# Optimization experiments

Measured on AMD Instinct MI355X. Metric: run time of the kernel, lower is better.

Reference implementation:

```python
import jax, jax.numpy as jnp
import numpy as np

B, D_IN, D_HID, D_OUT, N_EXP, K = 32768, 256, 512, 256, 16, 2


def setup_inputs() -> dict:
    key = jax.random.key(0)
    ks = jax.random.split(key, 5)
    s_in = 1.0 / np.sqrt(D_IN)
    s_hid = 1.0 / np.sqrt(D_HID)
    return {
        "x": jax.random.normal(ks[0], (B, D_IN), jnp.float32),
        "Wg": jax.random.normal(ks[1], (D_IN, N_EXP), jnp.float32) * s_in,
        "bg": jnp.zeros((N_EXP,), jnp.float32),
        "W1": jax.random.normal(ks[2], (N_EXP, D_IN, D_HID), jnp.float32) * s_in,
        "b1": jnp.zeros((N_EXP, D_HID), jnp.float32),
        "W2": jax.random.normal(ks[3], (N_EXP, D_HID, D_OUT), jnp.float32) * s_hid,
        "b2": jnp.zeros((N_EXP, D_OUT), jnp.float32),
    }


def reference(x, Wg, bg, W1, b1, W2, b2):
    # Gating: linear -> softmax -> top-k -> renormalize (inference path, no noise)
    logits = x @ Wg + bg                       # [B, E]
    probs = jax.nn.softmax(logits, axis=-1)
    top_w, top_idx = jax.lax.top_k(probs, K)   # [B, K]
    top_w = top_w / jnp.sum(top_w, axis=-1, keepdims=True)

    # Expert MLPs (evaluate all experts densely, then gather selected outputs;
    # same math as masked gather -> MLP -> weighted scatter-add)
    h = jax.nn.relu(jnp.einsum('bi,eih->beh', x, W1) + b1[None])  # [B, E, H]
    y_all = jnp.einsum('beh,eho->beo', h, W2) + b2[None]          # [B, E, O]

    y_sel = jnp.take_along_axis(y_all, top_idx[:, :, None], axis=1)  # [B, K, O]
    return jnp.sum(y_sel * top_w[:, :, None], axis=1)                # [B, O]
```

## Files before the change

kernel.cpp:

```cpp
#include <hip/hip_runtime.h>
#include <stdint.h>

#define BTOK 32768
#define DIN 256
#define DHID 512
#define DOUT 256
#define NEXP 16
#define BM 128
#define CH 64
#define NCH 8
#define SLOTS 96

typedef __attribute__((ext_vector_type(8))) short bf16x8;
typedef __attribute__((ext_vector_type(16))) float f32x16;

__device__ __forceinline__ unsigned short f2bf(float f){
  unsigned u = __builtin_bit_cast(unsigned, f);
  u = u + 0x7FFFu + ((u >> 16) & 1u);
  return (unsigned short)(u >> 16);
}
__device__ __forceinline__ float bf2f(unsigned short h){
  return __builtin_bit_cast(float, (unsigned)h << 16);
}
__device__ __forceinline__ void gload16(const void* g, void* l){
  __builtin_amdgcn_global_load_lds((const __attribute__((address_space(1))) unsigned int*)g,
                                   (__attribute__((address_space(3))) unsigned int*)l, 16, 0, 0);
}

__global__ __launch_bounds__(256) void transpose_cvt(const float* __restrict__ src,
                                                     unsigned short* __restrict__ dst,
                                                     int R, int C){
  __shared__ float t[32][33];
  int e = blockIdx.z, r0 = blockIdx.y * 32, c0 = blockIdx.x * 32;
  int lx = threadIdx.x & 31, ly = threadIdx.x >> 5;
  const float* s = src + (size_t)e * R * C;
  unsigned short* d = dst + (size_t)e * R * C;
#pragma unroll
  for (int i = 0; i < 4; i++){ int r = ly + i * 8; t[r][lx] = s[(size_t)(r0 + r) * C + c0 + lx]; }
  __syncthreads();
#pragma unroll
  for (int i = 0; i < 4; i++){ int r = ly + i * 8; d[(size_t)(c0 + r) * R + r0 + lx] = f2bf(t[lx][r]); }
}

__global__ __launch_bounds__(256) void transpose_cvt_w2(const float* __restrict__ src,
                                                        unsigned short* __restrict__ dst){
  __shared__ float t[32][33];
  int e = blockIdx.z, r0 = blockIdx.y * 32, c0 = blockIdx.x * 32;
  int lx = threadIdx.x & 31, ly = threadIdx.x >> 5;
  const float* s = src + (size_t)e * DHID * DOUT;
  unsigned short* d = dst + (size_t)e * DHID * DOUT + (r0 >> 6) * (DOUT * CH) + (r0 & 32);
#pragma unroll
  for (int i = 0; i < 4; i++){ int r = ly + i * 8; t[r][lx] = s[(size_t)(r0 + r) * DOUT + c0 + lx]; }
  __syncthreads();
#pragma unroll
  for (int i = 0; i < 4; i++){ int rr = ly + i * 8; d[(size_t)(c0 + rr) * CH + lx] = f2bf(t[lx][rr]); }
}

__global__ __launch_bounds__(256) void gating_kernel(const float* __restrict__ x,
                                                     const float* __restrict__ Wg,
                                                     const float* __restrict__ bg,
                                                     unsigned short* __restrict__ x_bf,
                                                     int* __restrict__ top_idx,
                                                     float* __restrict__ top_w,
                                                     int* __restrict__ counts){
  __shared__ float WgT[16][256];
  __shared__ int hist[16];
  int tid = threadIdx.x;
#pragma unroll
  for (int j = 0; j < 4; j++){
    float4 wv = *(const float4*)(Wg + tid * 16 + j * 4);
    WgT[j * 4 + 0][tid] = wv.x; WgT[j * 4 + 1][tid] = wv.y;
    WgT[j * 4 + 2][tid] = wv.z; WgT[j * 4 + 3][tid] = wv.w;
  }
  if (tid < 16) hist[tid] = 0;
  __syncthreads();
  int wid = tid >> 6, lane = tid & 63;

  for (int t = 0; t < 16; t++){
    int tok = blockIdx.x * 64 + wid * 16 + t;
    const float4 xv = *(const float4*)(x + (size_t)tok * DIN + lane * 4);
    ushort4 xb; xb.x = f2bf(xv.x); xb.y = f2bf(xv.y); xb.z = f2bf(xv.z); xb.w = f2bf(xv.w);
    *(ushort4*)(x_bf + (size_t)tok * DIN + lane * 4) = xb;
    float logit[16];
#pragma unroll
    for (int e = 0; e < 16; e++){
      const float4 wv = *(const float4*)(&WgT[e][lane * 4]);
      float v = xv.x * wv.x + xv.y * wv.y + xv.z * wv.z + xv.w * wv.w;
#pragma unroll
      for (int off = 32; off; off >>= 1) v += __shfl_xor(v, off, 64);
      logit[e] = v + bg[e];
    }
    if (lane == 0){
      int i1 = 0; float v1 = logit[0];
#pragma unroll
      for (int e = 1; e < 16; e++) if (logit[e] > v1){ v1 = logit[e]; i1 = e; }
      int i2 = -1; float v2 = -3.4e38f;
#pragma unroll
      for (int e = 0; e < 16; e++) if (e != i1 && logit[e] > v2){ v2 = logit[e]; i2 = e; }
      float tt = expf(v2 - v1);
      float w1 = 1.0f / (1.0f + tt);
      float w2 = tt / (1.0f + tt);
      top_idx[tok * 2] = i1; top_idx[tok * 2 + 1] = i2;
      top_w[tok * 2] = w1;  top_w[tok * 2 + 1] = w2;
      atomicAdd(&hist[i1], 1); atomicAdd(&hist[i2], 1);
    }
  }
  __syncthreads();
  if (tid < 16) atomicAdd(&counts[tid], hist[tid]);
}

__global__ void prefix_kernel(const int* __restrict__ counts, int* __restrict__ offsets,
                              int* __restrict__ cursor, int* __restrict__ bm_e,
                              int* __restrict__ bm_start, int* __restrict__ bm_end){
  int lane = threadIdx.x & 63;
  int c = (lane < 16) ? counts[lane] : 0;
  int s = c;
#pragma unroll
  for (int off = 1; off < 16; off <<= 1){ int o = __shfl_up(s, off, 64); if (lane >= off) s += o; }
  int start = s - c;
  if (lane < 16){ offsets[lane] = start; cursor[lane] = start; }
  int nb = (c + BM - 1) >> 7;
  int nb_partner = __shfl(nb, lane ^ 8, 64);
  if (lane < 8){
    int filled = nb + nb_partner;
    if (filled > SLOTS) filled = SLOTS;
    for (int i = filled; i < SLOTS; i++) bm_e[lane * SLOTS + i] = -1;
  }
  if (lane < 16){
    int sbase = (lane < 8) ? 0 : nb_partner;
    int xcd = lane & 7;
    for (int b = 0; b < nb; b++){
      int idx = xcd * SLOTS + sbase + b;
      if (sbase + b < SLOTS){
        bm_e[idx] = lane; bm_start[idx] = start + b * BM; bm_end[idx] = start + c;
      }
    }
  }
}

__global__ __launch_bounds__(256) void scatter_kernel(const int* __restrict__ top_idx,
                                                      const float* __restrict__ top_w,
                                                      int* __restrict__ cursor,
                                                      int* __restrict__ pair_tok,
                                                      float* __restrict__ pair_w){
  __shared__ int hist[16], base[16], rank[16];
  int tid = threadIdx.x;
  if (tid < 16){ hist[tid] = 0; rank[tid] = 0; }
  __syncthreads();
  int t = blockIdx.x * 256 + tid;
  int e0 = top_idx[t * 2], e1 = top_idx[t * 2 + 1];
  float w0 = top_w[t * 2], w1 = top_w[t * 2 + 1];
  atomicAdd(&hist[e0], 1); atomicAdd(&hist[e1], 1);
  __syncthreads();
  if (tid < 16) base[tid] = atomicAdd(&cursor[tid], hist[tid]);
  __syncthreads();
  int r0 = atomicAdd(&rank[e0], 1);
  int p0 = base[e0] + r0;
  pair_tok[p0] = t; pair_w[p0] = w0;
  int r1 = atomicAdd(&rank[e1], 1);
  int p1 = base[e1] + r1;
  pair_tok[p1] = t | (1 << 16); pair_w[p1] = w1;
}

__global__ __launch_bounds__(512, 1) void moe_gemm_kernel(
    const unsigned short* __restrict__ x_bf,
    const unsigned short* __restrict__ W1t,
    const unsigned short* __restrict__ W2c,
    const float* __restrict__ b1,
    const float* __restrict__ b2,
    const int* __restrict__ pair_tok, const float* __restrict__ pair_w,
    const int* __restrict__ bm_e, const int* __restrict__ bm_start,
    const int* __restrict__ bm_end,
    unsigned short* __restrict__ ypair){
  int xcd = blockIdx.x & 7, slot = blockIdx.x >> 3;
  int bmi = xcd * SLOTS + slot;
  int e = bm_e[bmi];
  if (e < 0) return;
  int rs = bm_start[bmi], re = bm_end[bmi];

  __shared__ unsigned short w1s[2][CH * 256];
  __shared__ unsigned short w2s[2][256 * CH];
  __shared__ unsigned short hs[BM * CH];

  int tid = threadIdx.x, wid = tid >> 6, lane = tid & 63;
  int l31 = lane & 31, l5 = lane >> 5;
  int mg = wid >> 1, hg = wid & 1;
  char* hsb = (char*)hs;
  const char* gW1 = (const char*)(W1t + (size_t)e * DHID * DIN);
  const char* gW2 = (const char*)(W2c + (size_t)e * DOUT * DHID);

  int o1, o2;
  { int r = tid >> 5; o1 = r * 512 + (((tid & 31) ^ (r & 15)) * 16); }
  { int p = tid >> 4; int q = (tid & 15) ^ (p & 15);
    o2 = (p * 2 + (q >> 3)) * 128 + (q & 7) * 16; }

#define STAGE(c, sl) {                                                    \
    const char* s1 = gW1 + (size_t)(c) * 32768;                           \
    const char* s2 = gW2 + (size_t)(c) * 32768;                           \
    char* d1 = (char*)w1s[sl]; char* d2 = (char*)w2s[sl];                 \
    _Pragma("unroll")                                                     \
    for (int k = 0; k < 4; k++){                                          \
      gload16(s1 + o1 + k * 8192, d1 + tid * 16 + k * 8192);              \
      gload16(s2 + o2 + k * 8192, d2 + tid * 16 + k * 8192);              \
    } }

  bf16x8 xr[16];
  {
    int g0 = rs + mg * 32 + l31;
    int gc = g0 < re ? g0 : (re - 1);
    int tok = pair_tok[gc] & 0xFFFF;
    const unsigned short* xrow = x_bf + (size_t)tok * DIN + l5 * 8;
#pragma unroll
    for (int ks = 0; ks < 16; ks++) xr[ks] = *(const bf16x8*)(xrow + ks * 16);
  }

  const f32x16 fzero = {0.f,0.f,0.f,0.f,0.f,0.f,0.f,0.f,0.f,0.f,0.f,0.f,0.f,0.f,0.f,0.f};
  f32x16 acc[4];
  acc[0] = fzero; acc[1] = fzero; acc[2] = fzero; acc[3] = fzero;

  STAGE(0, 0);
  asm volatile("s_waitcnt vmcnt(0)" ::: "memory");
  __builtin_amdgcn_sched_barrier(0);
  __builtin_amdgcn_s_barrier();
  __builtin_amdgcn_sched_barrier(0);

  int hid = hg * 32 + l31;
  int swzA = (hid & 15) << 4;

  for (int c = 0; c < NCH; c++){
    int sl = c & 1;
    if (c + 1 < NCH) STAGE(c + 1, sl ^ 1);

    float b1v = b1[e * DHID + c * CH + hid];

    {
      const char* w1b = (const char*)w1s[sl];
      f32x16 h0 = fzero, h1 = fzero;
#pragma unroll
      for (int ks = 0; ks < 16; ks += 2){
        bf16x8 bA = *(const bf16x8*)(w1b + hid * 512 + ((ks * 32 + l5 * 16) ^ swzA));
        bf16x8 bB = *(const bf16x8*)(w1b + hid * 512 + (((ks + 1) * 32 + l5 * 16) ^ swzA));
        h0 = __builtin_amdgcn_mfma_f32_32x32x16_bf16(xr[ks], bA, h0, 0, 0, 0);
        h1 = __builtin_amdgcn_mfma_f32_32x32x16_bf16(xr[ks + 1], bB, h1, 0, 0, 0);
      }
      f32x16 hsum = h0 + h1;
      int h2 = hg * 64 + l31 * 2;
#pragma unroll
      for (int r = 0; r < 16; r++){
        int tk = mg * 32 + (r & 3) + ((r >> 2) << 3) + (l5 << 2);
        float v = fmaxf(hsum[r] + b1v, 0.f);
        int adr = (tk >> 1) * 256 + ((((tk & 1) << 7) + h2) ^ (((tk >> 1) & 15) << 4));
        *(unsigned short*)(hsb + adr) = f2bf(v);
      }
    }
    asm volatile("s_waitcnt lgkmcnt(0)" ::: "memory");
    __builtin_amdgcn_sched_barrier(0);
    __builtin_amdgcn_s_barrier();
    __builtin_amdgcn_sched_barrier(0);

    {
      const char* w2b = (const char*)w2s[sl];
      int tk = mg * 32 + l31;
      int hswz = ((tk >> 1) & 15) << 4;
      int hbase = (tk >> 1) * 256;
      int hhi = (tk & 1) << 7;
#pragma unroll
      for (int ks = 0; ks < 4; ks++){
        bf16x8 ha = *(const bf16x8*)(hsb + hbase + ((hhi + ks * 32 + l5 * 16) ^ hswz));
#pragma unroll
        for (int ot = 0; ot < 4; ot++){
          int n = hg * 128 + ot * 32 + l31;
          int adr = (n >> 1) * 256 + ((((n & 1) << 7) + ks * 32 + l5 * 16) ^ (((n >> 1) & 15) << 4));
          bf16x8 bb = *(const bf16x8*)(w2b + adr);
          acc[ot] = __builtin_amdgcn_mfma_f32_32x32x16_bf16(ha, bb, acc[ot], 0, 0, 0);
        }
      }
    }
    if (c + 1 < NCH){
      asm volatile("s_waitcnt vmcnt(0) lgkmcnt(0)" ::: "memory");
      __builtin_amdgcn_sched_barrier(0);
      __builtin_amdgcn_s_barrier();
      __builtin_amdgcn_sched_barrier(0);
    }
  }

  {
    float b2v[4];
#pragma unroll
    for (int ot = 0; ot < 4; ot++) b2v[ot] = b2[e * DOUT + hg * 128 + ot * 32 + l31];
#pragma unroll
    for (int r = 0; r < 16; r++){
      int tl = mg * 32 + (r & 3) + ((r >> 2) << 3) + (l5 << 2);
      int gg = rs + tl;
      if (gg < re){
        int pt = pair_tok[gg];
        int yrow = (pt & 0xFFFF) * 2 + (pt >> 16);
        float w = pair_w[gg];
        unsigned short* yp = ypair + (size_t)yrow * DOUT + hg * 128 + l31;
#pragma unroll
        for (int ot = 0; ot < 4; ot++)
          yp[ot * 32] = f2bf(w * (acc[ot][r] + b2v[ot]));
      }
    }
  }
#undef STAGE
}

__global__ __launch_bounds__(256) void combine_kernel(const unsigned short* __restrict__ yp,
                                                      float* __restrict__ out){
  int idx = blockIdx.x * 256 + threadIdx.x;
  int t = idx >> 6;
  int c4 = (idx & 63) << 2;
  ushort4 a = *(const ushort4*)(yp + (size_t)(t * 2) * DOUT + c4);
  ushort4 b = *(const ushort4*)(yp + (size_t)(t * 2 + 1) * DOUT + c4);
  float4 o;
  o.x = bf2f(a.x) + bf2f(b.x);
  o.y = bf2f(a.y) + bf2f(b.y);
  o.z = bf2f(a.z) + bf2f(b.z);
  o.w = bf2f(a.w) + bf2f(b.w);
  *(float4*)(out + (size_t)t * DOUT + c4) = o;
}

extern "C" void kernel_launch(void* const* d_in, const int* in_sizes, int n_in,
                              void* d_out, int out_size, void* d_ws, size_t ws_size,
                              hipStream_t stream){
  (void)in_sizes; (void)n_in; (void)out_size; (void)ws_size;
  const float* x  = (const float*)d_in[0];
  const float* Wg = (const float*)d_in[1];
  const float* bg = (const float*)d_in[2];
  const float* W1 = (const float*)d_in[3];
  const float* b1 = (const float*)d_in[4];
  const float* W2 = (const float*)d_in[5];
  const float* b2 = (const float*)d_in[6];
  float* out = (float*)d_out;
  char* ws = (char*)d_ws;

  unsigned short* x_bf  = (unsigned short*)(ws);
  unsigned short* W1t   = (unsigned short*)(ws + 16777216);
  unsigned short* W2ck  = (unsigned short*)(ws + 20971520);
  unsigned short* ypair = (unsigned short*)(ws + 25165824);
  int*   top_idx  = (int*)  (ws + 58720256);
  float* top_w    = (float*)(ws + 58982400);
  int*   pair_tok = (int*)  (ws + 59244544);
  float* pair_w   = (float*)(ws + 59506688);
  int*   counts   = (int*)  (ws + 60030976);
  int*   offsets  = (int*)  (ws + 60031040);
  int*   cursor   = (int*)  (ws + 60031104);
  int*   bm_e     = (int*)  (ws + 60031232);
  int*   bm_start = (int*)  (ws + 60036608);
  int*   bm_end   = (int*)  (ws + 60041984);

  hipMemsetAsync(counts, 0, 64, stream);
  transpose_cvt<<<dim3(16, 8, 16), 256, 0, stream>>>(W1, W1t, 256, 512);
  transpose_cvt_w2<<<dim3(8, 16, 16), 256, 0, stream>>>(W2, W2ck);
  gating_kernel<<<512, 256, 0, stream>>>(x, Wg, bg, x_bf, top_idx, top_w, counts);
  prefix_kernel<<<1, 64, 0, stream>>>(counts, offsets, cursor, bm_e, bm_start, bm_end);
  scatter_kernel<<<128, 256, 0, stream>>>(top_idx, top_w, cursor, pair_tok, pair_w);
  moe_gemm_kernel<<<8 * SLOTS, 512, 0, stream>>>(x_bf, W1t, W2ck, b1, b2, pair_tok, pair_w,
                                                 bm_e, bm_start, bm_end, ypair);
  combine_kernel<<<8192, 256, 0, stream>>>(ypair, out);
}
```

Baseline: 159.5 us.

## Make MoE GEMM persistent with per-XCD atomic work queues

Replaces the fixed 768-block grid, where each block handled one slot and exited if empty, with a persistent grid of 256 blocks. Each block repeatedly claims the next 128-row tile from its own XCD's queue through an atomic counter, looping until that queue is drained. This avoids launching and retiring many empty or short-lived blocks and balances work dynamically within each XCD. In exchange it adds an atomic and a barrier per tile, serializes tiles within a block, and loses the overlap between blocks resident on the same CU.

```diff
diff --git a/kernel.cpp b/kernel.cpp
--- a/kernel.cpp
+++ b/kernel.cpp
@@ -111,7 +111,8 @@
 
 __global__ void prefix_kernel(const int* __restrict__ counts, int* __restrict__ offsets,
                               int* __restrict__ cursor, int* __restrict__ bm_e,
-                              int* __restrict__ bm_start, int* __restrict__ bm_end){
+                              int* __restrict__ bm_start, int* __restrict__ bm_end,
+                              int* __restrict__ xcd_cnt, int* __restrict__ xcd_cur){
   int lane = threadIdx.x & 63;
   int c = (lane < 16) ? counts[lane] : 0;
   int s = c;
@@ -124,7 +125,8 @@
   if (lane < 8){
     int filled = nb + nb_partner;
     if (filled > SLOTS) filled = SLOTS;
-    for (int i = filled; i < SLOTS; i++) bm_e[lane * SLOTS + i] = -1;
+    xcd_cnt[lane] = filled;
+    xcd_cur[lane] = 0;
   }
   if (lane < 16){
     int sbase = (lane < 8) ? 0 : nb_partner;
@@ -171,28 +173,39 @@
     const int* __restrict__ pair_tok, const float* __restrict__ pair_w,
     const int* __restrict__ bm_e, const int* __restrict__ bm_start,
     const int* __restrict__ bm_end,
+    int* __restrict__ xcd_cur, const int* __restrict__ xcd_cnt,
     unsigned short* __restrict__ ypair){
-  int xcd = blockIdx.x & 7, slot = blockIdx.x >> 3;
-  int bmi = xcd * SLOTS + slot;
-  int e = bm_e[bmi];
-  if (e < 0) return;
-  int rs = bm_start[bmi], re = bm_end[bmi];
+  int xcd = blockIdx.x & 7;
 
   __shared__ unsigned short w1s[2][CH * 256];
   __shared__ unsigned short w2s[2][256 * CH];
   __shared__ unsigned short hs[BM * CH];
+  __shared__ int s_u;
 
   int tid = threadIdx.x, wid = tid >> 6, lane = tid & 63;
   int l31 = lane & 31, l5 = lane >> 5;
   int mg = wid >> 1, hg = wid & 1;
   char* hsb = (char*)hs;
-  const char* gW1 = (const char*)(W1t + (size_t)e * DHID * DIN);
-  const char* gW2 = (const char*)(W2c + (size_t)e * DOUT * DHID);
 
   int o1, o2;
   { int r = tid >> 5; o1 = r * 512 + (((tid & 31) ^ (r & 15)) * 16); }
   { int p = tid >> 4; int q = (tid & 15) ^ (p & 15);
     o2 = (p * 2 + (q >> 3)) * 128 + (q & 7) * 16; }
+
+  int hid = hg * 32 + l31;
+  int swzA = (hid & 15) << 4;
+  const f32x16 fzero = {0.f,0.f,0.f,0.f,0.f,0.f,0.f,0.f,0.f,0.f,0.f,0.f,0.f,0.f,0.f,0.f};
+  int cnt = xcd_cnt[xcd];
+
+  for (;;){
+    if (tid == 0) s_u = atomicAdd(&xcd_cur[xcd], 1);
+    __syncthreads();
+    int u = s_u;
+    if (u >= cnt) break;
+    int bmi = xcd * SLOTS + u;
+    int e = bm_e[bmi], rs = bm_start[bmi], re = bm_end[bmi];
+    const char* gW1 = (const char*)(W1t + (size_t)e * DHID * DIN);
+    const char* gW2 = (const char*)(W2c + (size_t)e * DOUT * DHID);
 
 #define STAGE(c, sl) {                                                    \
     const char* s1 = gW1 + (size_t)(c) * 32768;                           \
@@ -204,106 +217,103 @@
       gload16(s2 + o2 + k * 8192, d2 + tid * 16 + k * 8192);              \
     } }
 
-  bf16x8 xr[16];
-  {
-    int g0 = rs + mg * 32 + l31;
-    int gc = g0 < re ? g0 : (re - 1);
-    int tok = pair_tok[gc] & 0xFFFF;
-    const unsigned short* xrow = x_bf + (size_t)tok * DIN + l5 * 8;
-#pragma unroll
-    for (int ks = 0; ks < 16; ks++) xr[ks] = *(const bf16x8*)(xrow + ks * 16);
-  }
-
-  const f32x16 fzero = {0.f,0.f,0.f,0.f,0.f,0.f,0.f,0.f,0.f,0.f,0.f,0.f,0.f,0.f,0.f,0.f};
-  f32x16 acc[4];
-  acc[0] = fzero; acc[1] = fzero; acc[2] = fzero; acc[3] = fzero;
-
-  STAGE(0, 0);
-  asm volatile("s_waitcnt vmcnt(0)" ::: "memory");
-  __builtin_amdgcn_sched_barrier(0);
-  __builtin_amdgcn_s_barrier();
-  __builtin_amdgcn_sched_barrier(0);
-
-  int hid = hg * 32 + l31;
-  int swzA = (hid & 15) << 4;
-
-  for (int c = 0; c < NCH; c++){
-    int sl = c & 1;
-    if (c + 1 < NCH) STAGE(c + 1, sl ^ 1);
-
-    float b1v = b1[e * DHID + c * CH + hid];
-
+    bf16x8 xr[16];
     {
-      const char* w1b = (const char*)w1s[sl];
-      f32x16 h0 = fzero, h1 = fzero;
-#pragma unroll
-      for (int ks = 0; ks < 16; ks += 2){
-        bf16x8 bA = *(const bf16x8*)(w1b + hid * 512 + ((ks * 32 + l5 * 16) ^ swzA));
-        bf16x8 bB = *(const bf16x8*)(w1b + hid * 512 + (((ks + 1) * 32 + l5 * 16) ^ swzA));
-        h0 = __builtin_amdgcn_mfma_f32_32x32x16_bf16(xr[ks], bA, h0, 0, 0, 0);
-        h1 = __builtin_amdgcn_mfma_f32_32x32x16_bf16(xr[ks + 1], bB, h1, 0, 0, 0);
-      }
-      f32x16 hsum = h0 + h1;
-      int h2 = hg * 64 + l31 * 2;
-#pragma unroll
-      for (int r = 0; r < 16; r++){
-        int tk = mg * 32 + (r & 3) + ((r >> 2) << 3) + (l5 << 2);
-        float v = fmaxf(hsum[r] + b1v, 0.f);
-        int adr = (tk >> 1) * 256 + ((((tk & 1) << 7) + h2) ^ (((tk >> 1) & 15) << 4));
-        *(unsigned short*)(hsb + adr) = f2bf(v);
-      }
-    }
-    asm volatile("s_waitcnt lgkmcnt(0)" ::: "memory");
+      int g0 = rs + mg * 32 + l31;
+      int gc = g0 < re ? g0 : (re - 1);
+      int tok = pair_tok[gc] & 0xFFFF;
+      const unsigned short* xrow = x_bf + (size_t)tok * DIN + l5 * 8;
+#pragma unroll
+      for (int ks = 0; ks < 16; ks++) xr[ks] = *(const bf16x8*)(xrow + ks * 16);
+    }
+
+    f32x16 acc[4];
+    acc[0] = fzero; acc[1] = fzero; acc[2] = fzero; acc[3] = fzero;
+
+    STAGE(0, 0);
+    asm volatile("s_waitcnt vmcnt(0)" ::: "memory");
     __builtin_amdgcn_sched_barrier(0);
     __builtin_amdgcn_s_barrier();
     __builtin_amdgcn_sched_barrier(0);
 
-    {
-      const char* w2b = (const char*)w2s[sl];
-      int tk = mg * 32 + l31;
-      int hswz = ((tk >> 1) & 15) << 4;
-      int hbase = (tk >> 1) * 256;
-      int hhi = (tk & 1) << 7;
-#pragma unroll
-      for (int ks = 0; ks < 4; ks++){
-        bf16x8 ha = *(const bf16x8*)(hsb + hbase + ((hhi + ks * 32 + l5 * 16) ^ hswz));
-#pragma unroll
-        for (int ot = 0; ot < 4; ot++){
-          int n = hg * 128 + ot * 32 + l31;
-          int adr = (n >> 1) * 256 + ((((n & 1) << 7) + ks * 32 + l5 * 16) ^ (((n >> 1) & 15) << 4));
-          bf16x8 bb = *(const bf16x8*)(w2b + adr);
-          acc[ot] = __builtin_amdgcn_mfma_f32_32x32x16_bf16(ha, bb, acc[ot], 0, 0, 0);
+    for (int c = 0; c < NCH; c++){
+      int sl = c & 1;
+      if (c + 1 < NCH) STAGE(c + 1, sl ^ 1);
+
+      float b1v = b1[e * DHID + c * CH + hid];
+
+      {
+        const char* w1b = (const char*)w1s[sl];
+        f32x16 h0 = fzero, h1 = fzero;
+#pragma unroll
+        for (int ks = 0; ks < 16; ks += 2){
+          bf16x8 bA = *(const bf16x8*)(w1b + hid * 512 + ((ks * 32 + l5 * 16) ^ swzA));
+          bf16x8 bB = *(const bf16x8*)(w1b + hid * 512 + (((ks + 1) * 32 + l5 * 16) ^ swzA));
+          h0 = __builtin_amdgcn_mfma_f32_32x32x16_bf16(xr[ks], bA, h0, 0, 0, 0);
+          h1 = __builtin_amdgcn_mfma_f32_32x32x16_bf16(xr[ks + 1], bB, h1, 0, 0, 0);
         }
-      }
-    }
-    if (c + 1 < NCH){
-      asm volatile("s_waitcnt vmcnt(0) lgkmcnt(0)" ::: "memory");
+        f32x16 hsum = h0 + h1;
+        int h2 = hg * 64 + l31 * 2;
+#pragma unroll
+        for (int r = 0; r < 16; r++){
+          int tk = mg * 32 + (r & 3) + ((r >> 2) << 3) + (l5 << 2);
+          float v = fmaxf(hsum[r] + b1v, 0.f);
+          int adr = (tk >> 1) * 256 + ((((tk & 1) << 7) + h2) ^ (((tk >> 1) & 15) << 4));
+          *(unsigned short*)(hsb + adr) = f2bf(v);
+        }
+      }
+      asm volatile("s_waitcnt lgkmcnt(0)" ::: "memory");
       __builtin_amdgcn_sched_barrier(0);
       __builtin_amdgcn_s_barrier();
       __builtin_amdgcn_sched_barrier(0);
-    }
-  }
-
-  {
-    float b2v[4];
-#pragma unroll
-    for (int ot = 0; ot < 4; ot++) b2v[ot] = b2[e * DOUT + hg * 128 + ot * 32 + l31];
-#pragma unroll
-    for (int r = 0; r < 16; r++){
-      int tl = mg * 32 + (r & 3) + ((r >> 2) << 3) + (l5 << 2);
-      int gg = rs + tl;
-      if (gg < re){
-        int pt = pair_tok[gg];
-        int yrow = (pt & 0xFFFF) * 2 + (pt >> 16);
-        float w = pair_w[gg];
-        unsigned short* yp = ypair + (size_t)yrow * DOUT + hg * 128 + l31;
-#pragma unroll
-        for (int ot = 0; ot < 4; ot++)
-          yp[ot * 32] = f2bf(w * (acc[ot][r] + b2v[ot]));
-      }
-    }
-  }
+
+      {
+        const char* w2b = (const char*)w2s[sl];
+        int tk = mg * 32 + l31;
+        int hswz = ((tk >> 1) & 15) << 4;
+        int hbase = (tk >> 1) * 256;
+        int hhi = (tk & 1) << 7;
+#pragma unroll
+        for (int ks = 0; ks < 4; ks++){
+          bf16x8 ha = *(const bf16x8*)(hsb + hbase + ((hhi + ks * 32 + l5 * 16) ^ hswz));
+#pragma unroll
+          for (int ot = 0; ot < 4; ot++){
+            int n = hg * 128 + ot * 32 + l31;
+            int adr = (n >> 1) * 256 + ((((n & 1) << 7) + ks * 32 + l5 * 16) ^ (((n >> 1) & 15) << 4));
+            bf16x8 bb = *(const bf16x8*)(w2b + adr);
+            acc[ot] = __builtin_amdgcn_mfma_f32_32x32x16_bf16(ha, bb, acc[ot], 0, 0, 0);
+          }
+        }
+      }
+      if (c + 1 < NCH){
+        asm volatile("s_waitcnt vmcnt(0) lgkmcnt(0)" ::: "memory");
+        __builtin_amdgcn_sched_barrier(0);
+        __builtin_amdgcn_s_barrier();
+        __builtin_amdgcn_sched_barrier(0);
+      }
+    }
+
+    {
+      float b2v[4];
+#pragma unroll
+      for (int ot = 0; ot < 4; ot++) b2v[ot] = b2[e * DOUT + hg * 128 + ot * 32 + l31];
+#pragma unroll
+      for (int r = 0; r < 16; r++){
+        int tl = mg * 32 + (r & 3) + ((r >> 2) << 3) + (l5 << 2);
+        int gg = rs + tl;
+        if (gg < re){
+          int pt = pair_tok[gg];
+          int yrow = (pt & 0xFFFF) * 2 + (pt >> 16);
+          float w = pair_w[gg];
+          unsigned short* yp = ypair + (size_t)yrow * DOUT + hg * 128 + l31;
+#pragma unroll
+          for (int ot = 0; ot < 4; ot++)
+            yp[ot * 32] = f2bf(w * (acc[ot][r] + b2v[ot]));
+        }
+      }
+    }
 #undef STAGE
+  }
 }
 
 __global__ __launch_bounds__(256) void combine_kernel(const unsigned short* __restrict__ yp,
@@ -349,14 +359,17 @@
   int*   bm_e     = (int*)  (ws + 60031232);
   int*   bm_start = (int*)  (ws + 60036608);
   int*   bm_end   = (int*)  (ws + 60041984);
+  int*   xcd_cnt  = (int*)  (ws + 60045184);
+  int*   xcd_cur  = (int*)  (ws + 60045248);
 
   hipMemsetAsync(counts, 0, 64, stream);
   transpose_cvt<<<dim3(16, 8, 16), 256, 0, stream>>>(W1, W1t, 256, 512);
   transpose_cvt_w2<<<dim3(8, 16, 16), 256, 0, stream>>>(W2, W2ck);
   gating_kernel<<<512, 256, 0, stream>>>(x, Wg, bg, x_bf, top_idx, top_w, counts);
-  prefix_kernel<<<1, 64, 0, stream>>>(counts, offsets, cursor, bm_e, bm_start, bm_end);
+  prefix_kernel<<<1, 64, 0, stream>>>(counts, offsets, cursor, bm_e, bm_start, bm_end,
+                                      xcd_cnt, xcd_cur);
   scatter_kernel<<<128, 256, 0, stream>>>(top_idx, top_w, cursor, pair_tok, pair_w);
-  moe_gemm_kernel<<<8 * SLOTS, 512, 0, stream>>>(x_bf, W1t, W2ck, b1, b2, pair_tok, pair_w,
-                                                 bm_e, bm_start, bm_end, ypair);
+  moe_gemm_kernel<<<256, 512, 0, stream>>>(x_bf, W1t, W2ck, b1, b2, pair_tok, pair_w,
+                                           bm_e, bm_start, bm_end, xcd_cur, xcd_cnt, ypair);
   combine_kernel<<<8192, 256, 0, stream>>>(ypair, out);
 }
```

Result: no change. 158.5 us (-0.6%).
